# Optimization experiments

Measured on AMD Instinct MI355X. Metric: run time of the kernel, lower is better.

The kernel has to match this reference:

```python
import jax, jax.numpy as jnp
import numpy as np

B = 512          # batch of graphs
N_LOCAL = 33     # local nodes per graph
NPG = 34         # nodes per graph (1 global + 33 local)
C = 768          # feat_dims[-1] (global feature channels)
FEAT = 1152      # concat_dim = sum(feat_dims) = 384 + 768
GPD = 2048       # global_proj_dim
HID = 1024       # hidden_dim_proj
H = 8            # num_heads
AD = 64          # att_dim
LLM = 4096       # llama_dim
DEG = 8          # average degree of random graph
E_PER = NPG * DEG
NT = B * NPG     # total nodes


def setup_inputs() -> dict:
    key = jax.random.key(0)
    ks = jax.random.split(key, 16)
    sc = 0.02
    local_features = jax.random.normal(ks[0], (B, 1, N_LOCAL, FEAT), jnp.float32)
    global_features = jax.random.normal(ks[1], (B, C, 8, 8, 4), jnp.float32)
    # random batched graph: edges stay within each graph, offset by 34*b
    src = jax.random.randint(ks[2], (B, E_PER), 0, NPG)
    dst = jax.random.randint(ks[3], (B, E_PER), 0, NPG)
    off = (jnp.arange(B, dtype=jnp.int32) * NPG)[:, None]
    edge_index = jnp.stack([(src + off).reshape(-1), (dst + off).reshape(-1)]).astype(jnp.int32)
    return {
        "local_features": local_features,
        "global_features": global_features,
        "edge_index": edge_index,
        "W1g": jax.random.normal(ks[4], (32 * C, GPD), jnp.float32) * sc,
        "b1g": jnp.zeros((GPD,), jnp.float32),
        "W2g": jax.random.normal(ks[5], (GPD, FEAT), jnp.float32) * sc,
        "b2g": jnp.zeros((FEAT,), jnp.float32),
        "Wp": jax.random.normal(ks[6], (FEAT, HID), jnp.float32) * sc,
        "bp": jnp.zeros((HID,), jnp.float32),
        "Wg": jax.random.normal(ks[7], (HID, H * AD), jnp.float32) * sc,
        "a_src": jax.random.normal(ks[8], (H, AD), jnp.float32) * sc,
        "a_dst": jax.random.normal(ks[9], (H, AD), jnp.float32) * sc,
        "Wllm": jax.random.normal(ks[10], (H * AD, LLM), jnp.float32) * sc,
        "bllm": jnp.zeros((LLM,), jnp.float32),
    }


def reference(local_features, global_features, edge_index,
              W1g, b1g, W2g, b2g, Wp, bp, Wg, a_src, a_dst, Wllm, bllm):
    # AdaptiveAvgPool3d((4,4,2)) on (8,8,4): exact 2x2x2 mean pooling
    x = global_features.reshape(B, C, 4, 2, 4, 2, 2, 2).mean(axis=(3, 5, 7))
    x = x.reshape(B, -1)                                   # [B, 32*C]
    out_global = jax.nn.relu(x @ W1g + b1g) @ W2g + b2g    # [B, FEAT]
    # concat global node with local nodes -> [B, 34, FEAT] -> flatten batched graph
    nodes = jnp.concatenate([out_global[:, None, :], local_features[:, 0]], axis=1)
    nodes = nodes.reshape(NT, FEAT)

    # GAT layer: hidden projection, per-head features, edge attention
    h = jax.nn.relu(nodes @ Wp + bp)                       # [NT, HID]
    z = (h @ Wg).reshape(NT, H, AD)                        # [NT, H, AD]
    s, d = edge_index[0], edge_index[1]
    e = jax.nn.leaky_relu(
        jnp.einsum('ehd,hd->eh', z[s], a_src) + jnp.einsum('ehd,hd->eh', z[d], a_dst),
        negative_slope=0.2)                                # [E, H]
    m = jax.ops.segment_max(e, d, num_segments=NT)
    m = jnp.where(jnp.isfinite(m), m, 0.0)                 # guard isolated nodes
    ex = jnp.exp(e - m[d])
    den = jax.ops.segment_sum(ex, d, num_segments=NT)
    alpha = ex / (den[d] + 1e-9)                           # neighbor softmax per dst
    agg = jax.ops.segment_sum(alpha[:, :, None] * z[s], d, num_segments=NT)  # [NT, H, AD]
    gnn_feats = agg.reshape(NT, H * AD)

    out = gnn_feats.reshape(B, NPG, H * AD) @ Wllm + bllm  # [B, 34, LLM]
    return out
```

## Files before the change

kernel.cpp:

```cpp
#include <hip/hip_runtime.h>
#include <hip/hip_bf16.h>
#include <math.h>

#define BB    512
#define NPG   34
#define NT    17408
#define FEAT  1152
#define GPD   2048
#define HID   1024
#define NH    8
#define AD    64
#define HA    512
#define LLM   4096
#define EPG   272
#define NE    139264
#define C32   24576
#define CC    768

#define AS3 __attribute__((address_space(3)))
#define AS1 __attribute__((address_space(1)))

typedef __attribute__((ext_vector_type(8))) short short8v;
typedef __attribute__((ext_vector_type(4))) float f32x4;

__device__ __forceinline__ ushort f2bf(float f) {
    __hip_bfloat16 h = __float2bfloat16(f);
    return __builtin_bit_cast(ushort, h);
}
__device__ __forceinline__ float bf2f(ushort u) {
    unsigned int x = ((unsigned int)u) << 16;
    return __builtin_bit_cast(float, x);
}

__device__ __forceinline__ void d_transpose64(const float* __restrict__ W, ushort* __restrict__ WT,
                                              int R, int Cn, int bx, int by,
                                              float (*tile)[65], int tid) {
    int c0 = bx * 64, r0 = by * 64;
    int rc = tid >> 6, cc = tid & 63;
#pragma unroll
    for (int i = 0; i < 16; i++) {
        int r = i * 4 + rc;
        tile[r][cc] = W[(size_t)(r0 + r) * Cn + c0 + cc];
    }
    __syncthreads();
#pragma unroll
    for (int i = 0; i < 2; i++) {
        int p = tid + i * 256;
        int c = p >> 3, ro = (p & 7) << 3;
        ushort u[8];
#pragma unroll
        for (int k = 0; k < 8; k++) u[k] = f2bf(tile[ro + k][c]);
        *(uint4*)&WT[(size_t)(c0 + c) * R + r0 + ro] = *(uint4*)u;
    }
}

__device__ __forceinline__ void d_pool(const float* __restrict__ gf, ushort* __restrict__ outB,
                                       int blk, int tid) {
    int t = blk * 256 + tid;
    int q = t & 15; int bc = t >> 4;
    int dO = q >> 2, hO = q & 3;
    const float* p = gf + (size_t)bc * 256 + dO * 64 + hO * 8;
    float4 r00 = *(const float4*)(p);
    float4 r01 = *(const float4*)(p + 4);
    float4 r10 = *(const float4*)(p + 32);
    float4 r11 = *(const float4*)(p + 36);
    float o0 = (r00.x + r00.y + r01.x + r01.y + r10.x + r10.y + r11.x + r11.y) * 0.125f;
    float o1 = (r00.z + r00.w + r01.z + r01.w + r10.z + r10.w + r11.z + r11.w) * 0.125f;
    int b = bc / CC, c = bc % CC;
    ushort2 v; v.x = f2bf(o0); v.y = f2bf(o1);
    *(ushort2*)(outB + (size_t)b * C32 + c * 32 + dO * 8 + hO * 2) = v;
}

__global__ __launch_bounds__(256) void k_prep(
    const float* __restrict__ W1g, ushort* __restrict__ W1gT,
    const float* __restrict__ W2g, ushort* __restrict__ W2gT,
    const float* __restrict__ Wp,  ushort* __restrict__ WpT,
    const float* __restrict__ Wg,  ushort* __restrict__ WgT,
    const float* __restrict__ Wllm, ushort* __restrict__ WllmT,
    const float* __restrict__ gf,  ushort* __restrict__ poolB) {
    __shared__ float tile[64][65];
    int blk = blockIdx.x, tid = threadIdx.x;
    if (blk < 12288) {
        d_transpose64(W1g, W1gT, C32, GPD, blk & 31, blk >> 5, tile, tid);
    } else if (blk < 12864) {
        int l = blk - 12288; d_transpose64(W2g, W2gT, GPD, FEAT, l % 18, l / 18, tile, tid);
    } else if (blk < 13152) {
        int l = blk - 12864; d_transpose64(Wp, WpT, FEAT, HID, l & 15, l >> 4, tile, tid);
    } else if (blk < 13280) {
        int l = blk - 13152; d_transpose64(Wg, WgT, HID, HA, l & 7, l >> 3, tile, tid);
    } else if (blk < 13792) {
        int l = blk - 13280; d_transpose64(Wllm, WllmT, HA, LLM, l & 63, l >> 6, tile, tid);
    } else {
        d_pool(gf, poolB, blk - 13792, tid);
    }
}

#define GLDS(gp, lp) __builtin_amdgcn_global_load_lds((const AS1 void*)(gp), (AS3 void*)(lp), 16, 0, 0)
#define STAGE_A(buf, h, tt) { \
    const ushort* s_ = gAs + (size_t)(tt) * 64 + (size_t)(2 * (h)) * rK; \
    ushort* d_ = lds + (buf) * 32768 + (2 * (h)) * 4096 + (w << 9); \
    GLDS(s_, d_); GLDS(s_ + rK, d_ + 4096); }
#define STAGE_B(buf, h, tt) { \
    const ushort* s_ = gBs + (size_t)(tt) * 64 + (size_t)(2 * (h)) * rK; \
    ushort* d_ = lds + (buf) * 32768 + 16384 + (2 * (h)) * 4096 + (w << 9); \
    GLDS(s_, d_); GLDS(s_ + rK, d_ + 4096); }
#define DSRA(BO, mh) { _Pragma("unroll") for (int mf = 0; mf < 4; mf++) { \
    const ushort* p_ = lds + (BO) + aBase + ((mh) * 64 + mf * 16) * 64; \
    aF[mf][0] = *(const short8v*)(p_ + k0s); \
    aF[mf][1] = *(const short8v*)(p_ + k1s); } }
#define DSRB(BO, nh, BF) { _Pragma("unroll") for (int nf = 0; nf < 2; nf++) { \
    const ushort* p_ = lds + (BO) + bBase + ((nh) * 32 + nf * 16) * 64; \
    BF[nf][0] = *(const short8v*)(p_ + k0s); \
    BF[nf][1] = *(const short8v*)(p_ + k1s); } }
#define MM(mh, nh, BF) { \
    asm volatile("s_waitcnt lgkmcnt(0)" ::: "memory"); \
    __builtin_amdgcn_sched_barrier(0); \
    __builtin_amdgcn_s_setprio(1); \
    _Pragma("unroll") for (int mf = 0; mf < 4; mf++) \
    _Pragma("unroll") for (int nf = 0; nf < 2; nf++) { \
        acc[(mh)*4+mf][(nh)*2+nf] = __builtin_amdgcn_mfma_f32_16x16x32_bf16(aF[mf][0], BF[nf][0], acc[(mh)*4+mf][(nh)*2+nf], 0, 0, 0); \
        acc[(mh)*4+mf][(nh)*2+nf] = __builtin_amdgcn_mfma_f32_16x16x32_bf16(aF[mf][1], BF[nf][1], acc[(mh)*4+mf][(nh)*2+nf], 0, 0, 0); } \
    __builtin_amdgcn_s_setprio(0); }
#define BAR __builtin_amdgcn_s_barrier()
#define VMW4 { asm volatile("s_waitcnt vmcnt(4)" ::: "memory"); __builtin_amdgcn_sched_barrier(0); }

template<bool SWZ, bool SPLITK, bool BIAS, bool RELU, bool OUTBF>
__global__ __launch_bounds__(512, 2) void k_gemm256(
    const ushort* __restrict__ A, const ushort* __restrict__ BT,
    const float* __restrict__ bias, void* __restrict__ Cout,
    int M, int N, int K, int kChunk) {
    __shared__ ushort lds[65536];
    const int t = threadIdx.x;
    const int w = t >> 6, l = t & 63;
    const int wm = w >> 2, wn = w & 3;
    int m0, n0;
    if (SWZ) {
        const int gx = gridDim.x;
        const int nwg = gx * gridDim.y;
        const int id = blockIdx.y * gx + blockIdx.x;
        const int qx = nwg >> 3, rx = nwg & 7;
        const int xcd = id & 7, pos = id >> 3;
        const int nid = (xcd < rx ? xcd * (qx + 1) : rx * (qx + 1) + (xcd - rx) * qx) + pos;
        m0 = (nid / gx) * 256; n0 = (nid % gx) * 256;
    } else {
        m0 = blockIdx.y * 256; n0 = blockIdx.x * 256;
    }
    const int kBase = SPLITK ? blockIdx.z * kChunk : 0;
    const int NTt = (SPLITK ? kChunk : K) / 64;

    const int rowLo = t >> 3;
    const int keSrc = ((t & 7) << 3) ^ (((rowLo >> 2) & 1) << 5) ^ (((rowLo >> 3) & 1) << 4);
    const ushort* gAs = A + (size_t)(m0 + rowLo) * K + kBase + keSrc;
    const ushort* gBs = BT + (size_t)(n0 + rowLo) * K + kBase + keSrc;
    const size_t rK = (size_t)64 * K;

    const int fcol = l & 15, fk = (l >> 4) << 3;
    const int flipR = (((l >> 2) & 1) << 5) | (((l >> 3) & 1) << 4);
    const int k0s = fk ^ flipR;
    const int k1s = fk ^ 32 ^ flipR;
    const int aBase = (wm * 128 + fcol) * 64;
    const int bBase = 16384 + (wn * 64 + fcol) * 64;

    short8v aF[4][2], bF0[2][2], bF1[2][2];
    f32x4 acc[8][4] = {};

    STAGE_B(0, 0, 0); STAGE_B(0, 1, 0); STAGE_A(0, 0, 0); STAGE_A(0, 1, 0);
    STAGE_B(1, 0, 1); STAGE_B(1, 1, 1);
    VMW4;
    BAR;

    const int NITER = NTt >> 1;
    for (int it = 0; it < NITER; ++it) {
        const int t1 = 2 * it + 1;
        const int t2r = 2 * it + 2, t3r = 2 * it + 3;
        const int t2 = t2r < NTt ? t2r : 0;
        const int t3 = t3r < NTt ? t3r : 0;
        DSRA(0, 0); DSRB(0, 0, bF0); STAGE_A(1, 0, t1);
        BAR; MM(0, 0, bF0); BAR;
        DSRB(0, 1, bF1); STAGE_A(1, 1, t1);
        BAR; MM(0, 1, bF1); BAR;
        DSRA(0, 1); STAGE_B(0, 0, t2);
        BAR; MM(1, 1, bF1); BAR;
        STAGE_B(0, 1, t2); VMW4;
        BAR; MM(1, 0, bF0); BAR;
        DSRA(32768, 0); DSRB(32768, 0, bF0); STAGE_A(0, 0, t2);
        BAR; MM(0, 0, bF0); BAR;
        DSRB(32768, 1, bF1); STAGE_A(0, 1, t2);
        BAR; MM(0, 1, bF1); BAR;
        DSRA(32768, 1); STAGE_B(1, 0, t3);
        BAR; MM(1, 1, bF1); BAR;
        STAGE_B(1, 1, t3); VMW4;
        BAR; MM(1, 0, bF0); BAR;
    }
    asm volatile("s_waitcnt vmcnt(0)" ::: "memory");
    BAR;

    const int orow = (l >> 4) << 2;
    float* eph = ((float*)lds) + w * 2176;
    const int ecol = (l & 15) << 2;
    const int erow4 = l >> 4;
#pragma unroll
    for (int pass = 0; pass < 4; pass++) {
#pragma unroll
        for (int mi = 0; mi < 2; mi++) {
            int mf = pass * 2 + mi;
#pragma unroll
            for (int nf = 0; nf < 4; nf++)
#pragma unroll
                for (int r = 0; r < 4; r++)
                    eph[(mi * 16 + orow + r) * 68 + nf * 16 + fcol] = acc[mf][nf][r];
        }
#pragma unroll
        for (int g = 0; g < 8; g++) {
            int lrow = g * 4 + erow4;
            f32x4 v = *(f32x4*)&eph[lrow * 68 + ecol];
            int row = m0 + wm * 128 + pass * 32 + lrow;
            int col = n0 + wn * 64 + ecol;
            if (BIAS) {
                float4 bb = *(const float4*)(bias + col);
                v[0] += bb.x; v[1] += bb.y; v[2] += bb.z; v[3] += bb.w;
            }
            if (RELU) {
#pragma unroll
                for (int q = 0; q < 4; q++) v[q] = v[q] > 0.f ? v[q] : 0.f;
            }
            size_t off = (size_t)row * N + col;
            if (SPLITK) off += (size_t)blockIdx.z * (size_t)M * N;
            if (OUTBF) {
                ushort4 u;
                u.x = f2bf(v[0]); u.y = f2bf(v[1]); u.z = f2bf(v[2]); u.w = f2bf(v[3]);
                *(ushort4*)&((ushort*)Cout)[off] = u;
            } else {
                float4 fv = {v[0], v[1], v[2], v[3]};
                *(float4*)&((float*)Cout)[off] = fv;
            }
        }
    }
}

template<bool SPLITK, bool BIAS, bool RELU, bool OUTBF>
__global__ __launch_bounds__(256) void k_gemm_bf(
    const ushort* __restrict__ A, const ushort* __restrict__ BT,
    const float* __restrict__ bias, void* __restrict__ Cout,
    int M, int N, int K, int kChunk) {
    __shared__ ushort lA[128 * 32];
    __shared__ ushort lB[128 * 32];
    const int t = threadIdx.x;
    const int w = t >> 6, l = t & 63;
    const int m0 = blockIdx.y * 128, n0 = blockIdx.x * 128;
    const int kLen = SPLITK ? kChunk : K;
    const int k0 = SPLITK ? blockIdx.z * kChunk : 0;
    const int srow = w * 16 + (l >> 2);
    const int skq = (l & 3) << 3;
    const ushort* gA = A + (size_t)(m0 + srow) * K + k0 + skq;
    const ushort* gB = BT + (size_t)(n0 + srow) * K + k0 + skq;
    ushort* lA0 = lA + w * 512;
    ushort* lB0 = lB + w * 512;
    const size_t str64 = (size_t)64 * K;
    const int wr = (w >> 1) << 6, wc = (w & 1) << 6;
    const int fcol = l & 15, fk = (l >> 4) << 3;

    f32x4 acc[4][4] = {};
    for (int kk = 0; kk < kLen; kk += 32) {
        __syncthreads();
        GLDS(gA + kk,         lA0);
        GLDS(gA + kk + str64, lA0 + 2048);
        GLDS(gB + kk,         lB0);
        GLDS(gB + kk + str64, lB0 + 2048);
        __syncthreads();
        short8v a[4], b[4];
#pragma unroll
        for (int f = 0; f < 4; f++) {
            a[f] = *(const short8v*)(lA + (wr + f * 16 + fcol) * 32 + fk);
            b[f] = *(const short8v*)(lB + (wc + f * 16 + fcol) * 32 + fk);
        }
#pragma unroll
        for (int i = 0; i < 4; i++)
#pragma unroll
            for (int j = 0; j < 4; j++)
                acc[i][j] = __builtin_amdgcn_mfma_f32_16x16x32_bf16(a[i], b[j], acc[i][j], 0, 0, 0);
    }
    const int orow = (l >> 4) << 2;
#pragma unroll
    for (int i = 0; i < 4; i++) {
#pragma unroll
        for (int j = 0; j < 4; j++) {
            int col = n0 + wc + j * 16 + fcol;
            float bv = BIAS ? bias[col] : 0.f;
#pragma unroll
            for (int r = 0; r < 4; r++) {
                int row = m0 + wr + i * 16 + orow + r;
                float v = acc[i][j][r] + bv;
                if (RELU) v = v > 0.f ? v : 0.f;
                if (OUTBF) {
                    ((ushort*)Cout)[(size_t)row * N + col] = f2bf(v);
                } else {
                    size_t off = (size_t)row * N + col;
                    if (SPLITK) off += (size_t)blockIdx.z * (size_t)M * N;
                    ((float*)Cout)[off] = v;
                }
            }
        }
    }
}

__global__ __launch_bounds__(256) void k_red1(const ushort* __restrict__ part,
                                              const float* __restrict__ b1g,
                                              ushort* __restrict__ g1B) {
    int i8 = (blockIdx.x * 256 + threadIdx.x) * 8;
    float v[8];
#pragma unroll
    for (int k = 0; k < 8; k++) v[k] = b1g[(i8 + k) & (GPD - 1)];
#pragma unroll
    for (int q = 0; q < 16; q++) {
        uint4 pk = *(const uint4*)(part + (size_t)q * 1048576 + i8);
        const ushort* pu = (const ushort*)&pk;
#pragma unroll
        for (int k = 0; k < 8; k++) v[k] += bf2f(pu[k]);
    }
    ushort u[8];
#pragma unroll
    for (int k = 0; k < 8; k++) u[k] = f2bf(v[k] > 0.f ? v[k] : 0.f);
    *(uint4*)&g1B[i8] = *(uint4*)u;
}

__global__ __launch_bounds__(256) void k_nodes(const float* __restrict__ part2,
                                               const float* __restrict__ b2g,
                                               const float* __restrict__ locf,
                                               ushort* __restrict__ nodesB) {
    int idx = blockIdx.x * 256 + threadIdx.x;
    int node = idx / 144, cc = idx - node * 144;
    int b = node / NPG, j = node - b * NPG;
    int c = cc * 8;
    ushort* dst = nodesB + (size_t)node * FEAT + c;
    if (j == 0) {
        float v[8];
        float4 b0 = *(const float4*)(b2g + c), b1 = *(const float4*)(b2g + c + 4);
        v[0] = b0.x; v[1] = b0.y; v[2] = b0.z; v[3] = b0.w;
        v[4] = b1.x; v[5] = b1.y; v[6] = b1.z; v[7] = b1.w;
#pragma unroll
        for (int q = 0; q < 4; q++) {
            const float* pp = part2 + (size_t)q * 589824 + (size_t)b * FEAT + c;
            float4 p0 = *(const float4*)pp, p1 = *(const float4*)(pp + 4);
            v[0] += p0.x; v[1] += p0.y; v[2] += p0.z; v[3] += p0.w;
            v[4] += p1.x; v[5] += p1.y; v[6] += p1.z; v[7] += p1.w;
        }
        ushort u[8];
#pragma unroll
        for (int k = 0; k < 8; k++) u[k] = f2bf(v[k]);
        *(uint4*)dst = *(uint4*)u;
    } else {
        const float* s = locf + ((size_t)b * 33 + (j - 1)) * FEAT + c;
        float4 v0 = *(const float4*)s, v1 = *(const float4*)(s + 4);
        ushort u[8] = {f2bf(v0.x), f2bf(v0.y), f2bf(v0.z), f2bf(v0.w),
                       f2bf(v1.x), f2bf(v1.y), f2bf(v1.z), f2bf(v1.w)};
        *(uint4*)dst = *(uint4*)u;
    }
}

__global__ __launch_bounds__(512) void k_gat(const int* __restrict__ es, const int* __restrict__ ed,
                                             const float* __restrict__ z,
                                             const float* __restrict__ a_src,
                                             const float* __restrict__ a_dst,
                                             ushort* __restrict__ gnnB) {
    __shared__ float zt[NPG][520];
    __shared__ float sps[NPG][NH], spd[NPG][NH], sm[NPG][NH], sden[NPG][NH];
    __shared__ float esc[EPG][NH];
    __shared__ int srcl[EPG], dll[EPG], order[EPG], cnt[NPG], bstart[NPG + 1];
    int b = blockIdx.x, t = threadIdx.x;
    for (int i = t; i < NPG * 128; i += 512) {
        int n = i >> 7, c4 = (i & 127) << 2;
        *(float4*)&zt[n][c4] = *(const float4*)&z[((size_t)b * NPG + n) * HA + c4];
    }
    for (int e = t; e < EPG; e += 512) {
        srcl[e] = es[b * EPG + e] - b * NPG;
        dll[e]  = ed[b * EPG + e] - b * NPG;
    }
    if (t < NPG) cnt[t] = 0;
    __syncthreads();
    {
        int wv = t >> 6, l = t & 63;
        for (int n = wv; n < NPG; n += 8) {
            float s[NH], d[NH];
#pragma unroll
            for (int i = 0; i < NH; i++) {
                float zv = zt[n][i * 64 + l];
                s[i] = zv * a_src[i * 64 + l];
                d[i] = zv * a_dst[i * 64 + l];
            }
#pragma unroll
            for (int i = 0; i < NH; i++) {
#pragma unroll
                for (int off = 32; off > 0; off >>= 1) {
                    s[i] += __shfl_xor(s[i], off);
                    d[i] += __shfl_xor(d[i], off);
                }
            }
            if (l == 0) {
#pragma unroll
                for (int i = 0; i < NH; i++) { sps[n][i] = s[i]; spd[n][i] = d[i]; }
            }
        }
    }
    for (int e = t; e < EPG; e += 512) atomicAdd(&cnt[dll[e]], 1);
    __syncthreads();
    if (t == 0) {
        int s = 0;
        for (int n = 0; n < NPG; n++) { bstart[n] = s; s += cnt[n]; }
        bstart[NPG] = s;
    }
    __syncthreads();
    if (t < EPG) {
        int myd = dll[t];
        int rank = 0;
        for (int e2 = 0; e2 < EPG; e2++) {
            int d2 = dll[e2];
            rank += (e2 < t && d2 == myd) ? 1 : 0;
        }
        order[bstart[myd] + rank] = t;
    }
    __syncthreads();
    for (int i = t; i < EPG * NH; i += 512) {
        int e = i >> 3, h = i & 7;
        float sc = sps[srcl[e]][h] + spd[dll[e]][h];
        esc[e][h] = sc > 0.f ? sc : 0.2f * sc;
    }
    __syncthreads();
    for (int i = t; i < NPG * NH; i += 512) {
        int n = i >> 3, h = i & 7;
        float m = -INFINITY;
        for (int j = bstart[n]; j < bstart[n + 1]; j++) m = fmaxf(m, esc[order[j]][h]);
        if (m == -INFINITY) m = 0.f;
        float den = 0.f;
        for (int j = bstart[n]; j < bstart[n + 1]; j++) den += expf(esc[order[j]][h] - m);
        sm[n][h] = m; sden[n][h] = den;
    }
    __syncthreads();
    for (int i = t; i < EPG * NH; i += 512) {
        int e = i >> 3, h = i & 7;
        esc[e][h] = expf(esc[e][h] - sm[dll[e]][h]) / (sden[dll[e]][h] + 1e-9f);
    }
    __syncthreads();
    for (int c = t; c < NPG * 64; c += 512) {
        int n = c >> 6, rem = c & 63, h = rem >> 3, d0 = (rem & 7) << 3;
        float acc[8] = {};
        for (int j = bstart[n]; j < bstart[n + 1]; j++) {
            int e = order[j];
            float a = esc[e][h];
            const float* zp = &zt[srcl[e]][h * 64 + d0];
#pragma unroll
            for (int q = 0; q < 8; q++) acc[q] = fmaf(a, zp[q], acc[q]);
        }
        ushort u[8];
#pragma unroll
        for (int q = 0; q < 8; q++) u[q] = f2bf(acc[q]);
        *(uint4*)&gnnB[((size_t)b * NPG + n) * HA + h * 64 + d0] = *(uint4*)u;
    }
}

extern "C" void kernel_launch(void* const* d_in, const int* in_sizes, int n_in,
                              void* d_out, int out_size, void* d_ws, size_t ws_size,
                              hipStream_t stream) {
    const float* locf  = (const float*)d_in[0];
    const float* gf    = (const float*)d_in[1];
    const int*   ei    = (const int*)d_in[2];
    const float* W1g   = (const float*)d_in[3];
    const float* b1g   = (const float*)d_in[4];
    const float* W2g   = (const float*)d_in[5];
    const float* b2g   = (const float*)d_in[6];
    const float* Wp    = (const float*)d_in[7];
    const float* bp    = (const float*)d_in[8];
    const float* Wg    = (const float*)d_in[9];
    const float* a_src = (const float*)d_in[10];
    const float* a_dst = (const float*)d_in[11];
    const float* Wllm  = (const float*)d_in[12];
    const float* bllm  = (const float*)d_in[13];
    float* out = (float*)d_out;
    float* ws  = (float*)d_ws;
    const int* es = ei;
    const int* ed = ei + NE;

    float*  z      = out;
    ushort* W1gT   = (ushort*)(out + 8912896);
    ushort* hB     = (ushort*)(out + 8912896);
    ushort* poolB  = (ushort*)(out + 34078720);
    ushort* part1B = (ushort*)(out + 40370176);
    ushort* nodesB = (ushort*)(out + 40370176);
    ushort* g1B    = (ushort*)(out + 57147392);
    ushort* W2gT   = (ushort*)(out + 57671680);
    ushort* WpT    = (ushort*)(out + 58851328);
    ushort* WgT    = (ushort*)(out + 59441152);
    float*  part2  = out + 59998208;
    ushort* WllmT = (ushort*)ws;
    ushort* gnnB  = (ushort*)(ws + 1048576);

    k_prep<<<38368, 256, 0, stream>>>(W1g, W1gT, W2g, W2gT, Wp, WpT, Wg, WgT,
                                      Wllm, WllmT, gf, poolB);
    k_gemm256<false, true, false, false, true><<<dim3(8, 2, 16), 512, 0, stream>>>(
        poolB, W1gT, nullptr, part1B, 512, GPD, C32, 1536);
    k_red1<<<512, 256, 0, stream>>>(part1B, b1g, g1B);
    k_gemm_bf<true, false, false, false><<<dim3(9, 4, 4), 256, 0, stream>>>(
        g1B, W2gT, nullptr, part2, 512, FEAT, GPD, 512);
    k_nodes<<<9792, 256, 0, stream>>>(part2, b2g, locf, nodesB);
    k_gemm256<true, false, true, true, true><<<dim3(4, 68), 512, 0, stream>>>(
        nodesB, WpT, bp, hB, NT, HID, FEAT, 0);
    k_gemm256<true, false, false, false, false><<<dim3(2, 68), 512, 0, stream>>>(
        hB, WgT, nullptr, z, NT, HA, HID, 0);
    k_gat<<<BB, 512, 0, stream>>>(es, ed, z, a_src, a_dst, gnnB);
    k_gemm256<true, false, true, false, false><<<dim3(16, 68), 512, 0, stream>>>(
        gnnB, WllmT, bllm, out, NT, LLM, HA, 0);
}
```

Baseline: 541.3 us.

## Add nontemporal stores, bf16 z output, smaller-tile Wg GEMM, deeper split-K for W2g

Adds a template flag to the 256-tile GEMM that writes outputs with nontemporal stores. It is enabled for the split-K W1g partials and the final LLM projection, so large write-once outputs do not pollute the cache. The Wg projection now runs on the 128-tile GEMM with more blocks and writes z in bf16, and the GAT kernel converts it back on load, which halves z traffic at some precision cost. The W2g split-K goes from 4 to 8 chunks for more parallelism, at the price of reducing more partials in k_nodes.

```diff
diff --git a/kernel.cpp b/kernel.cpp
--- a/kernel.cpp
+++ b/kernel.cpp
@@ -22,6 +22,7 @@
 
 typedef __attribute__((ext_vector_type(8))) short short8v;
 typedef __attribute__((ext_vector_type(4))) float f32x4;
+typedef __attribute__((ext_vector_type(4))) ushort u16x4;
 
 __device__ __forceinline__ ushort f2bf(float f) {
     __hip_bfloat16 h = __float2bfloat16(f);
@@ -124,7 +125,7 @@
 #define BAR __builtin_amdgcn_s_barrier()
 #define VMW4 { asm volatile("s_waitcnt vmcnt(4)" ::: "memory"); __builtin_amdgcn_sched_barrier(0); }
 
-template<bool SWZ, bool SPLITK, bool BIAS, bool RELU, bool OUTBF>
+template<bool SWZ, bool SPLITK, bool BIAS, bool RELU, bool OUTBF, bool NTST>
 __global__ __launch_bounds__(512, 2) void k_gemm256(
     const ushort* __restrict__ A, const ushort* __restrict__ BT,
     const float* __restrict__ bias, void* __restrict__ Cout,
@@ -227,12 +228,13 @@
             size_t off = (size_t)row * N + col;
             if (SPLITK) off += (size_t)blockIdx.z * (size_t)M * N;
             if (OUTBF) {
-                ushort4 u;
-                u.x = f2bf(v[0]); u.y = f2bf(v[1]); u.z = f2bf(v[2]); u.w = f2bf(v[3]);
-                *(ushort4*)&((ushort*)Cout)[off] = u;
+                u16x4 u;
+                u[0] = f2bf(v[0]); u[1] = f2bf(v[1]); u[2] = f2bf(v[2]); u[3] = f2bf(v[3]);
+                if (NTST) __builtin_nontemporal_store(u, (u16x4*)&((ushort*)Cout)[off]);
+                else      *(u16x4*)&((ushort*)Cout)[off] = u;
             } else {
-                float4 fv = {v[0], v[1], v[2], v[3]};
-                *(float4*)&((float*)Cout)[off] = fv;
+                if (NTST) __builtin_nontemporal_store(v, (f32x4*)&((float*)Cout)[off]);
+                else      *(f32x4*)&((float*)Cout)[off] = v;
             }
         }
     }
@@ -339,7 +341,7 @@
         v[0] = b0.x; v[1] = b0.y; v[2] = b0.z; v[3] = b0.w;
         v[4] = b1.x; v[5] = b1.y; v[6] = b1.z; v[7] = b1.w;
 #pragma unroll
-        for (int q = 0; q < 4; q++) {
+        for (int q = 0; q < 8; q++) {
             const float* pp = part2 + (size_t)q * 589824 + (size_t)b * FEAT + c;
             float4 p0 = *(const float4*)pp, p1 = *(const float4*)(pp + 4);
             v[0] += p0.x; v[1] += p0.y; v[2] += p0.z; v[3] += p0.w;
@@ -359,7 +361,7 @@
 }
 
 __global__ __launch_bounds__(512) void k_gat(const int* __restrict__ es, const int* __restrict__ ed,
-                                             const float* __restrict__ z,
+                                             const ushort* __restrict__ zB,
                                              const float* __restrict__ a_src,
                                              const float* __restrict__ a_dst,
                                              ushort* __restrict__ gnnB) {
@@ -368,9 +370,12 @@
     __shared__ float esc[EPG][NH];
     __shared__ int srcl[EPG], dll[EPG], order[EPG], cnt[NPG], bstart[NPG + 1];
     int b = blockIdx.x, t = threadIdx.x;
-    for (int i = t; i < NPG * 128; i += 512) {
-        int n = i >> 7, c4 = (i & 127) << 2;
-        *(float4*)&zt[n][c4] = *(const float4*)&z[((size_t)b * NPG + n) * HA + c4];
+    for (int i = t; i < NPG * 64; i += 512) {
+        int n = i >> 6, c0 = (i & 63) << 3;
+        uint4 pk = *(const uint4*)&zB[((size_t)b * NPG + n) * HA + c0];
+        const ushort* pu = (const ushort*)&pk;
+#pragma unroll
+        for (int q = 0; q < 8; q++) zt[n][c0 + q] = bf2f(pu[q]);
     }
     for (int e = t; e < EPG; e += 512) {
         srcl[e] = es[b * EPG + e] - b * NPG;
@@ -480,7 +485,7 @@
     const int* es = ei;
     const int* ed = ei + NE;
 
-    float*  z      = out;
+    ushort* zB     = (ushort*)out;
     ushort* W1gT   = (ushort*)(out + 8912896);
     ushort* hB     = (ushort*)(out + 8912896);
     ushort* poolB  = (ushort*)(out + 34078720);
@@ -496,17 +501,17 @@
 
     k_prep<<<38368, 256, 0, stream>>>(W1g, W1gT, W2g, W2gT, Wp, WpT, Wg, WgT,
                                       Wllm, WllmT, gf, poolB);
-    k_gemm256<false, true, false, false, true><<<dim3(8, 2, 16), 512, 0, stream>>>(
+    k_gemm256<false, true, false, false, true, true><<<dim3(8, 2, 16), 512, 0, stream>>>(
         poolB, W1gT, nullptr, part1B, 512, GPD, C32, 1536);
     k_red1<<<512, 256, 0, stream>>>(part1B, b1g, g1B);
-    k_gemm_bf<true, false, false, false><<<dim3(9, 4, 4), 256, 0, stream>>>(
-        g1B, W2gT, nullptr, part2, 512, FEAT, GPD, 512);
+    k_gemm_bf<true, false, false, false><<<dim3(9, 4, 8), 256, 0, stream>>>(
+        g1B, W2gT, nullptr, part2, 512, FEAT, GPD, 256);
     k_nodes<<<9792, 256, 0, stream>>>(part2, b2g, locf, nodesB);
-    k_gemm256<true, false, true, true, true><<<dim3(4, 68), 512, 0, stream>>>(
+    k_gemm256<true, false, true, true, true, false><<<dim3(4, 68), 512, 0, stream>>>(
         nodesB, WpT, bp, hB, NT, HID, FEAT, 0);
-    k_gemm256<true, false, false, false, false><<<dim3(2, 68), 512, 0, stream>>>(
-        hB, WgT, nullptr, z, NT, HA, HID, 0);
-    k_gat<<<BB, 512, 0, stream>>>(es, ed, z, a_src, a_dst, gnnB);
-    k_gemm256<true, false, true, false, false><<<dim3(16, 68), 512, 0, stream>>>(
+    k_gemm_bf<false, false, false, true><<<dim3(4, 136), 256, 0, stream>>>(
+        hB, WgT, nullptr, zB, NT, HA, HID, 0);
+    k_gat<<<BB, 512, 0, stream>>>(es, ed, zB, a_src, a_dst, gnnB);
+    k_gemm256<true, false, true, false, false, true><<<dim3(16, 68), 512, 0, stream>>>(
         gnnB, WllmT, bllm, out, NT, LLM, HA, 0);
 }
```

Result: faster. 527.0 us (-2.6%).
